# Optimization experiments

Hardware: AMD Instinct MI355X
Metric: run time of the kernel (lower is better)

The kernel has to match this reference:

```python
import jax, jax.numpy as jnp
import numpy as np

DIM = 768
N_HEADS = 12
HEAD_DIM = DIM // N_HEADS
HIDDEN = int(DIM * 4.0)
EPS = 1e-6


def setup_inputs() -> dict:
    key = jax.random.key(0)
    ks = jax.random.split(key, 12)
    s = 0.02
    return {
        "x": jax.random.normal(ks[0], (4, 2048, DIM), dtype=jnp.float32),
        "ln1_g": jnp.ones((DIM,), jnp.float32),
        "ln1_b": jnp.zeros((DIM,), jnp.float32),
        "qkv_w": jax.random.normal(ks[1], (3 * DIM, DIM), jnp.float32) * s,
        "qkv_b": jnp.zeros((3 * DIM,), jnp.float32),
        "proj_w": jax.random.normal(ks[2], (DIM, DIM), jnp.float32) * s,
        "proj_b": jnp.zeros((DIM,), jnp.float32),
        "ln2_g": jnp.ones((DIM,), jnp.float32),
        "ln2_b": jnp.zeros((DIM,), jnp.float32),
        "fc1_w": jax.random.normal(ks[3], (HIDDEN, DIM), jnp.float32) * s,
        "fc1_b": jnp.zeros((HIDDEN,), jnp.float32),
        "fc2_w": jax.random.normal(ks[4], (DIM, HIDDEN), jnp.float32) * s,
        "fc2_b": jnp.zeros((DIM,), jnp.float32),
    }


def layer_norm(x, g, b):
    mu = jnp.mean(x, axis=-1, keepdims=True)
    var = jnp.mean(jnp.square(x - mu), axis=-1, keepdims=True)
    return (x - mu) * jax.lax.rsqrt(var + EPS) * g + b


def reference(x, ln1_g, ln1_b, qkv_w, qkv_b, proj_w, proj_b,
              ln2_g, ln2_b, fc1_w, fc1_b, fc2_w, fc2_b):
    B, N, D = x.shape
    # --- attention branch ---
    h = layer_norm(x, ln1_g, ln1_b)
    qkv = h @ qkv_w.T + qkv_b                      # [B, N, 3D]
    qkv = qkv.reshape(B, N, 3, N_HEADS, HEAD_DIM).transpose(2, 0, 3, 1, 4)
    q, k, v = qkv[0], qkv[1], qkv[2]               # each [B, H, N, d]
    scale = HEAD_DIM ** -0.5
    scores = jnp.einsum("bhqd,bhkd->bhqk", q, k) * scale
    attn = jax.nn.softmax(scores, axis=-1)
    out = jnp.einsum("bhqk,bhkd->bhqd", attn, v)   # [B, H, N, d]
    out = out.transpose(0, 2, 1, 3).reshape(B, N, D)
    x = x + (out @ proj_w.T + proj_b)
    # --- MLP branch ---
    h = layer_norm(x, ln2_g, ln2_b)
    h = jax.nn.gelu(h @ fc1_w.T + fc1_b, approximate=False)
    x = x + (h @ fc2_w.T + fc2_b)
    return x
```

## Files before the change

### kernel.cpp

```cpp
#include <hip/hip_runtime.h>


#define DIM    768
#define NHEAD  12
#define HDIM   64
#define HID    3072
#define BATCH  4
#define SEQ    2048
#define MTOT   (BATCH * SEQ)
#define D3     (3 * DIM)

#define QSCALE 0.18033688011112042f
#define GELU_K 2.30220816f

typedef short bf16x8 __attribute__((ext_vector_type(8)));
typedef float f32x4  __attribute__((ext_vector_type(4)));

__device__ __forceinline__ float exp2fast(float x) {
    return __builtin_amdgcn_exp2f(x);
}

__device__ __forceinline__ float gelu_f(float v) {
    float y = v * (1.f + 0.044715f * v * v) * GELU_K;
    float t = exp2fast(fminf(y, 30.f));
#if __has_builtin(__builtin_amdgcn_rcpf)
    return v * t * __builtin_amdgcn_rcpf(t + 1.f);
#else
    return v * t / (t + 1.f);
#endif
}

__device__ __forceinline__ short f2bf(float f) {
    union { float f; unsigned u; } c; c.f = f;
    unsigned r = c.u + 0x7FFFu + ((c.u >> 16) & 1u);
    return (short)(r >> 16);
}

__device__ __forceinline__ short4 pk4bf(float a, float b, float c, float d) {
    int lo, hi;
    asm("v_cvt_pk_bf16_f32 %0, %1, %2" : "=v"(lo) : "v"(a), "v"(b));
    asm("v_cvt_pk_bf16_f32 %0, %1, %2" : "=v"(hi) : "v"(c), "v"(d));
    short4 r;
    *(int*)&r.x = lo; *(int*)&r.z = hi;
    return r;
}

__device__ __forceinline__ void gld_lds16(const short* g, short* l) {
    __builtin_amdgcn_global_load_lds(
        (const __attribute__((address_space(1))) unsigned int*)g,
        (__attribute__((address_space(3))) unsigned int*)l, 16, 0, 0);
}

__global__ __launch_bounds__(256) void tobf4_k(
    const float* __restrict__ s0, short* __restrict__ d0, int n0,
    const float* __restrict__ s1, short* __restrict__ d1, int n1,
    const float* __restrict__ s2, short* __restrict__ d2, int n2,
    const float* __restrict__ s3, short* __restrict__ d3, int n3)
{
    int i = blockIdx.x * 256 + threadIdx.x;
    const float* s; short* d;
    if (i < n0)                { s = s0; d = d0; }
    else if ((i -= n0) < n1)   { s = s1; d = d1; }
    else if ((i -= n1) < n2)   { s = s2; d = d2; }
    else if ((i -= n2) < n3)   { s = s3; d = d3; }
    else return;
    float4 v = ((const float4*)s)[i];
    ((short4*)d)[i] = pk4bf(v.x, v.y, v.z, v.w);
}

__global__ __launch_bounds__(256) void ln_k(
    const float* __restrict__ x, const float* __restrict__ g,
    const float* __restrict__ bta, short* __restrict__ y)
{
    __shared__ float sb[2][4];
    const int row = blockIdx.x, tid = threadIdx.x;
    const float* xr = x + (size_t)row * DIM;
    float v0 = xr[tid], v1 = xr[tid + 256], v2 = xr[tid + 512];
    float s = v0 + v1 + v2;
    #pragma unroll
    for (int o = 32; o; o >>= 1) s += __shfl_down(s, o);
    if ((tid & 63) == 0) sb[0][tid >> 6] = s;
    __syncthreads();
    float mu = (sb[0][0] + sb[0][1] + sb[0][2] + sb[0][3]) * (1.f / DIM);
    float d0 = v0 - mu, d1 = v1 - mu, d2 = v2 - mu;
    float q = d0 * d0 + d1 * d1 + d2 * d2;
    #pragma unroll
    for (int o = 32; o; o >>= 1) q += __shfl_down(q, o);
    if ((tid & 63) == 0) sb[1][tid >> 6] = q;
    __syncthreads();
    float var = (sb[1][0] + sb[1][1] + sb[1][2] + sb[1][3]) * (1.f / DIM);
    float inv = rsqrtf(var + 1e-6f);
    short* yr = y + (size_t)row * DIM;
    yr[tid]       = f2bf(d0 * inv * g[tid]       + bta[tid]);
    yr[tid + 256] = f2bf(d1 * inv * g[tid + 256] + bta[tid + 256]);
    yr[tid + 512] = f2bf(d2 * inv * g[tid + 512] + bta[tid + 512]);
}

template<int MODE>
__global__ __launch_bounds__(512) void gemmA_k(
    const short* __restrict__ A, const short* __restrict__ W,
    const float* __restrict__ bias,
    void* __restrict__ Cout, short* __restrict__ vt,
    int M, int N, int K)
{
    __shared__ __align__(16) short sm[2][28672];

    const int tid = threadIdx.x, lane = tid & 63, wv = tid >> 6;
    const int l15 = lane & 15, quad = lane >> 4;

    const int gx = gridDim.x;
    const int bid = blockIdx.y * gx + blockIdx.x;
    const int bm = (bid / gx) << 8;
    const int bn = (bid % gx) * 192;

    const int srow  = lane >> 3;
    const int chunk = (lane & 7) ^ srow;
    const int arow  = wv * 8 + srow;

    const short* Ag = A + (size_t)(bm + arow) * K + chunk * 8;
    const short* Wg = W + (size_t)(bn + arow) * K + chunk * 8;

    const int nt = K >> 6;

    auto stage = [&](short* s_, int k0) {
        #pragma unroll
        for (int i = 0; i < 4; ++i)
            gld_lds16(Ag + k0 + (size_t)(i * 64) * K,
                      s_ + i * 4096 + wv * 512);
        #pragma unroll
        for (int i = 0; i < 3; ++i)
            gld_lds16(Wg + k0 + (size_t)(i * 64) * K,
                      s_ + 16384 + i * 4096 + wv * 512);
    };

    f32x4 acc[4][6] = {};
    stage(&sm[0][0], 0);

    const int rsel = (wv >> 1) * 64;
    const int csel = (wv & 1) * 96;
    const int xorr = (l15 & 7) << 4;

    for (int t = 0; t < nt; ++t) {
        const char* Sc = (const char*)&sm[t & 1][0];
        asm volatile("s_waitcnt vmcnt(0)" ::: "memory");
        __builtin_amdgcn_s_barrier();
        __builtin_amdgcn_sched_barrier(0);
        if (t + 1 < nt) stage(&sm[(t + 1) & 1][0], (t + 1) << 6);

        #pragma unroll
        for (int ks = 0; ks < 2; ++ks) {
            bf16x8 af[4], bfr[6];
            const int kc = ((ks << 6) + (quad << 4)) ^ xorr;
            #pragma unroll
            for (int mf = 0; mf < 4; ++mf) {
                const int row = rsel + mf * 16 + l15;
                af[mf] = *(const bf16x8*)(Sc + (row << 7) + kc);
            }
            #pragma unroll
            for (int nf = 0; nf < 6; ++nf) {
                const int brow = csel + nf * 16 + l15;
                bfr[nf] = *(const bf16x8*)(Sc + 32768 + (brow << 7) + kc);
            }
            __builtin_amdgcn_s_setprio(1);
            #pragma unroll
            for (int mf = 0; mf < 4; ++mf)
                #pragma unroll
                for (int nf = 0; nf < 6; ++nf)
                    acc[mf][nf] = __builtin_amdgcn_mfma_f32_16x16x32_bf16(
                        af[mf], bfr[nf], acc[mf][nf], 0, 0, 0);
            __builtin_amdgcn_s_setprio(0);
        }
    }

    if (MODE == 3 && bn >= 1536) {
        const size_t bbase = (size_t)(bm >> 11) * NHEAD;
        #pragma unroll
        for (int nf = 0; nf < 6; ++nf) {
            const int col = bn + csel + nf * 16 + l15;
            const float bv = bias[col];
            const int d = col - 1536, hh = d >> 6, dd = d & 63;
            const size_t vrow = (((bbase + hh) << 6) + dd) * SEQ;
            #pragma unroll
            for (int mf = 0; mf < 4; ++mf) {
                const int n0 = (bm & 2047) + rsel + mf * 16 + (quad << 2);
                *(short4*)&vt[vrow + n0] =
                    pk4bf(acc[mf][nf][0] + bv, acc[mf][nf][1] + bv,
                          acc[mf][nf][2] + bv, acc[mf][nf][3] + bv);
            }
        }
        return;
    }

    #pragma unroll
    for (int nf = 0; nf < 6; ++nf) {
        const int col = bn + csel + nf * 16 + l15;
        const float bv = bias[col];
        #pragma unroll
        for (int mf = 0; mf < 4; ++mf) {
            const int row0 = bm + rsel + mf * 16 + (quad << 2);
            #pragma unroll
            for (int r = 0; r < 4; ++r) {
                float v = acc[mf][nf][r] + bv;
                const size_t idx = (size_t)(row0 + r) * N + col;
                if (MODE == 2) {
                    ((short*)Cout)[idx] = f2bf(gelu_f(v));
                } else {
                    if (col < DIM) v *= QSCALE;
                    ((short*)Cout)[idx] = f2bf(v);
                }
            }
        }
    }
}

template<int MODE>
__global__ __launch_bounds__(512) void gemm8_k(
    const short* __restrict__ A, const short* __restrict__ W,
    const float* __restrict__ bias, const float* __restrict__ resid,
    void* __restrict__ Cout, short* __restrict__ vt,
    int M, int N, int K)
{
    __shared__ __align__(16) short sm[3][20480];

    const int tid = threadIdx.x, lane = tid & 63, wv = tid >> 6;
    const int l15 = lane & 15, quad = lane >> 4;

    const int gx = gridDim.x;
    const int bid = blockIdx.y * gx + blockIdx.x;
    const int s = bid >> 3, xcd = bid & 7;
    const int st = ((s >> 5) << 3) + xcd;
    const int cell = s & 31, cy = cell >> 2, cx = cell & 3;
    const int nstx = gx >> 2;
    const int sty = st / nstx, stx = st - sty * nstx;
    const int bm = (((sty << 3) + cy) << 7);
    const int bn = ((stx << 2) + cx) * 192;

    const int srow  = lane >> 3;
    const int chunk = (lane & 7) ^ srow;
    const int arow  = wv * 8 + srow;

    const short* Ag = A + (size_t)(bm + arow) * K + chunk * 8;
    const short* Wg = W + (size_t)(bn + arow) * K + chunk * 8;

    const int nt = K >> 6;

    auto stage = [&](short* s_, int k0) {
        #pragma unroll
        for (int i = 0; i < 2; ++i)
            gld_lds16(Ag + k0 + (size_t)(i * 64) * K,
                      s_ + i * 4096 + wv * 512);
        #pragma unroll
        for (int i = 0; i < 3; ++i)
            gld_lds16(Wg + k0 + (size_t)(i * 64) * K,
                      s_ + 8192 + i * 4096 + wv * 512);
    };

    f32x4 acc[4][3] = {};
    stage(&sm[0][0], 0);
    stage(&sm[1][0], (nt > 1 ? 1 : 0) << 6);

    const int rsel = (wv >> 2) * 64;
    const int csel = (wv & 3) * 48;
    const int xorr = (l15 & 7) << 4;

    for (int t = 0; t < nt; ++t) {
        const char* Sc = (const char*)&sm[t % 3][0];
        asm volatile("s_waitcnt vmcnt(5)" ::: "memory");
        __builtin_amdgcn_s_barrier();
        __builtin_amdgcn_sched_barrier(0);
        const int kn = (t + 2 < nt ? t + 2 : nt - 1) << 6;
        stage(&sm[(t + 2) % 3][0], kn);

        #pragma unroll
        for (int ks = 0; ks < 2; ++ks) {
            bf16x8 af[4], bfr[3];
            const int kc = ((ks << 6) + (quad << 4)) ^ xorr;
            #pragma unroll
            for (int mf = 0; mf < 4; ++mf) {
                const int row = rsel + mf * 16 + l15;
                af[mf] = *(const bf16x8*)(Sc + (row << 7) + kc);
            }
            #pragma unroll
            for (int nf = 0; nf < 3; ++nf) {
                const int brow = csel + nf * 16 + l15;
                bfr[nf] = *(const bf16x8*)(Sc + 16384 + (brow << 7) + kc);
            }
            __builtin_amdgcn_s_setprio(1);
            #pragma unroll
            for (int mf = 0; mf < 4; ++mf)
                #pragma unroll
                for (int nf = 0; nf < 3; ++nf)
                    acc[mf][nf] = __builtin_amdgcn_mfma_f32_16x16x32_bf16(
                        af[mf], bfr[nf], acc[mf][nf], 0, 0, 0);
            __builtin_amdgcn_s_setprio(0);
        }
    }

    #pragma unroll
    for (int nf = 0; nf < 3; ++nf) {
        const int col = bn + csel + nf * 16 + l15;
        const float bv = bias[col];
        #pragma unroll
        for (int mf = 0; mf < 4; ++mf) {
            const int row0 = bm + rsel + mf * 16 + (quad << 2);
            #pragma unroll
            for (int r = 0; r < 4; ++r) {
                float v = acc[mf][nf][r] + bv;
                const size_t idx = (size_t)(row0 + r) * N + col;
                ((float*)Cout)[idx] = v + resid[idx];
            }
        }
    }
}

__global__ __launch_bounds__(256) void attn_k(
    const short* __restrict__ qkv, const short* __restrict__ vt,
    short* __restrict__ out)
{
    __shared__ __align__(16) short Ks[64][64];
    __shared__ __align__(16) short Vs[64][64];
    __shared__ __align__(16) short Ps[4][32][64];

    const int bh = blockIdx.x, b = bh / NHEAD, h = bh % NHEAD;
    const int qb = blockIdx.y;
    const int tid = threadIdx.x, lane = tid & 63, wv = tid >> 6;
    const int l15 = lane & 15, quad = lane >> 4;
    const int lsw = (l15 & 7) << 3;

    const size_t qbase = (size_t)b * SEQ * D3;
    const size_t vbase = (((size_t)bh) << 6) * SEQ;

    bf16x8 qf[2][2];
    #pragma unroll
    for (int tm = 0; tm < 2; ++tm) {
        const int m = (qb << 7) + wv * 32 + tm * 16 + l15;
        #pragma unroll
        for (int ks = 0; ks < 2; ++ks)
            qf[tm][ks] = *(const bf16x8*)&qkv[qbase + (size_t)m * D3 + h * HDIM
                                             + ks * 32 + (quad << 3)];
    }

    float psum[2] = {0.f, 0.f};
    f32x4 acc[2][4] = {};

    const int srow = tid >> 3;
    const int scol = (tid & 7) << 3;

    for (int kb = 0; kb < SEQ / 64; ++kb) {
        __syncthreads();
        #pragma unroll
        for (int p = 0; p < 2; ++p) {
            const int r = srow + p * 32;
            const int pc = scol ^ ((r & 7) << 3);
            *(int4*)&Ks[r][pc] = *(const int4*)&qkv[qbase
                + (size_t)((kb << 6) + r) * D3 + DIM + h * HDIM + scol];
            *(int4*)&Vs[r][pc] = *(const int4*)&vt[vbase
                + (size_t)r * SEQ + (kb << 6) + scol];
        }
        __syncthreads();

        f32x4 st[2][4] = {};
        __builtin_amdgcn_s_setprio(1);
        #pragma unroll
        for (int kt = 0; kt < 4; ++kt)
            #pragma unroll
            for (int ks = 0; ks < 2; ++ks) {
                bf16x8 kf = *(const bf16x8*)
                    &Ks[kt * 16 + l15][(ks * 32 + (quad << 3)) ^ lsw];
                #pragma unroll
                for (int tm = 0; tm < 2; ++tm)
                    st[tm][kt] = __builtin_amdgcn_mfma_f32_16x16x32_bf16(
                        kf, qf[tm][ks], st[tm][kt], 0, 0, 0);
            }
        __builtin_amdgcn_s_setprio(0);

        #pragma unroll
        for (int tm = 0; tm < 2; ++tm) {
            #pragma unroll
            for (int kt = 0; kt < 4; ++kt) {
                const float p0 = exp2fast(st[tm][kt][0]);
                const float p1 = exp2fast(st[tm][kt][1]);
                const float p2 = exp2fast(st[tm][kt][2]);
                const float p3 = exp2fast(st[tm][kt][3]);
                psum[tm] += (p0 + p1) + (p2 + p3);
                *(short4*)&Ps[wv][tm * 16 + l15]
                             [(kt * 16 + (quad << 2)) ^ lsw] =
                    pk4bf(p0, p1, p2, p3);
            }
        }

        #pragma unroll
        for (int ks = 0; ks < 2; ++ks) {
            bf16x8 pf[2];
            #pragma unroll
            for (int tm = 0; tm < 2; ++tm)
                pf[tm] = *(const bf16x8*)
                    &Ps[wv][tm * 16 + l15][(ks * 32 + (quad << 3)) ^ lsw];
            __builtin_amdgcn_s_setprio(1);
            #pragma unroll
            for (int u = 0; u < 4; ++u) {
                bf16x8 vf = *(const bf16x8*)
                    &Vs[u * 16 + l15][(ks * 32 + (quad << 3)) ^ lsw];
                #pragma unroll
                for (int tm = 0; tm < 2; ++tm)
                    acc[tm][u] = __builtin_amdgcn_mfma_f32_16x16x32_bf16(
                        vf, pf[tm], acc[tm][u], 0, 0, 0);
            }
            __builtin_amdgcn_s_setprio(0);
        }
    }

    #pragma unroll
    for (int tm = 0; tm < 2; ++tm) {
        psum[tm] += __shfl_xor(psum[tm], 16);
        psum[tm] += __shfl_xor(psum[tm], 32);
    }

    #pragma unroll
    for (int tm = 0; tm < 2; ++tm) {
        const float inv = 1.f / psum[tm];
        const int q = (qb << 7) + wv * 32 + tm * 16 + l15;
        #pragma unroll
        for (int u = 0; u < 4; ++u) {
            const int d0 = u * 16 + (quad << 2);
            *(short4*)&out[((size_t)b * SEQ + q) * DIM + h * HDIM + d0] =
                pk4bf(acc[tm][u][0] * inv, acc[tm][u][1] * inv,
                      acc[tm][u][2] * inv, acc[tm][u][3] * inv);
        }
    }
}

extern "C" void kernel_launch(void* const* d_in, const int* in_sizes, int n_in,
                              void* d_out, int out_size, void* d_ws, size_t ws_size,
                              hipStream_t stream) {
    const float* x      = (const float*)d_in[0];
    const float* ln1_g  = (const float*)d_in[1];
    const float* ln1_b  = (const float*)d_in[2];
    const float* qkv_w  = (const float*)d_in[3];
    const float* qkv_b  = (const float*)d_in[4];
    const float* proj_w = (const float*)d_in[5];
    const float* proj_b = (const float*)d_in[6];
    const float* ln2_g  = (const float*)d_in[7];
    const float* ln2_b  = (const float*)d_in[8];
    const float* fc1_w  = (const float*)d_in[9];
    const float* fc1_b  = (const float*)d_in[10];
    const float* fc2_w  = (const float*)d_in[11];
    const float* fc2_b  = (const float*)d_in[12];
    float* out = (float*)d_out;

    short* ws16 = (short*)d_ws;
    short* wqkv = ws16;
    short* wprj = wqkv + (size_t)D3 * DIM;
    short* wf1  = wprj + (size_t)DIM * DIM;
    short* wf2  = wf1  + (size_t)HID * DIM;
    short* h    = wf2  + (size_t)DIM * HID;
    short* big  = h    + (size_t)MTOT * DIM;
    short* vtb  = big  + (size_t)MTOT * HID;
    float* x2   = (float*)(vtb + (size_t)MTOT * DIM);

    dim3 blk(256);

    const int n0 = (D3 * DIM) / 4, n1 = (DIM * DIM) / 4,
              n2 = (HID * DIM) / 4, n3 = (DIM * HID) / 4;
    tobf4_k<<<(n0 + n1 + n2 + n3 + 255) / 256, blk, 0, stream>>>(
        qkv_w, wqkv, n0, proj_w, wprj, n1, fc1_w, wf1, n2, fc2_w, wf2, n3);

    ln_k<<<MTOT, blk, 0, stream>>>(x, ln1_g, ln1_b, h);
    gemmA_k<3><<<dim3(D3 / 192, MTOT / 256), 512, 0, stream>>>(
        h, wqkv, qkv_b, big, vtb, MTOT, D3, DIM);
    attn_k<<<dim3(BATCH * NHEAD, SEQ / 128), blk, 0, stream>>>(big, vtb, h);
    gemm8_k<0><<<dim3(DIM / 192, MTOT / 128), 512, 0, stream>>>(
        h, wprj, proj_b, x, x2, nullptr, MTOT, DIM, DIM);
    ln_k<<<MTOT, blk, 0, stream>>>(x2, ln2_g, ln2_b, vtb);
    gemmA_k<2><<<dim3(HID / 192, MTOT / 256), 512, 0, stream>>>(
        vtb, wf1, fc1_b, big, nullptr, MTOT, HID, DIM);
    gemm8_k<0><<<dim3(DIM / 192, MTOT / 128), 512, 0, stream>>>(
        big, wf2, fc2_b, x2, out, nullptr, MTOT, DIM, HID);
}
```

Before: 354.4 us.

## Switch GEMM to double-buffered LDS and register-prefetch attention K/V tiles

```diff
diff --git a/kernel.cpp b/kernel.cpp
--- a/kernel.cpp
+++ b/kernel.cpp
@@ -214,13 +214,13 @@
 }
 
 template<int MODE>
-__global__ __launch_bounds__(512) void gemm8_k(
+__global__ __launch_bounds__(512, 4) void gemm8_k(
     const short* __restrict__ A, const short* __restrict__ W,
     const float* __restrict__ bias, const float* __restrict__ resid,
     void* __restrict__ Cout, short* __restrict__ vt,
     int M, int N, int K)
 {
-    __shared__ __align__(16) short sm[3][20480];
+    __shared__ __align__(16) short sm[2][20480];
 
     const int tid = threadIdx.x, lane = tid & 63, wv = tid >> 6;
     const int l15 = lane & 15, quad = lane >> 4;
@@ -257,19 +257,17 @@
 
     f32x4 acc[4][3] = {};
     stage(&sm[0][0], 0);
-    stage(&sm[1][0], (nt > 1 ? 1 : 0) << 6);
 
     const int rsel = (wv >> 2) * 64;
     const int csel = (wv & 3) * 48;
     const int xorr = (l15 & 7) << 4;
 
     for (int t = 0; t < nt; ++t) {
-        const char* Sc = (const char*)&sm[t % 3][0];
-        asm volatile("s_waitcnt vmcnt(5)" ::: "memory");
+        const char* Sc = (const char*)&sm[t & 1][0];
+        asm volatile("s_waitcnt vmcnt(0)" ::: "memory");
         __builtin_amdgcn_s_barrier();
         __builtin_amdgcn_sched_barrier(0);
-        const int kn = (t + 2 < nt ? t + 2 : nt - 1) << 6;
-        stage(&sm[(t + 2) % 3][0], kn);
+        if (t + 1 < nt) stage(&sm[(t + 1) & 1][0], (t + 1) << 6);
 
         #pragma unroll
         for (int ks = 0; ks < 2; ++ks) {
@@ -346,16 +344,34 @@
     const int srow = tid >> 3;
     const int scol = (tid & 7) << 3;
 
+    int4 kreg[2], vreg[2];
+    #pragma unroll
+    for (int p = 0; p < 2; ++p) {
+        const int r = srow + p * 32;
+        kreg[p] = *(const int4*)&qkv[qbase + (size_t)r * D3 + DIM
+                                     + h * HDIM + scol];
+        vreg[p] = *(const int4*)&vt[vbase + (size_t)r * SEQ + scol];
+    }
+
     for (int kb = 0; kb < SEQ / 64; ++kb) {
         __syncthreads();
         #pragma unroll
         for (int p = 0; p < 2; ++p) {
             const int r = srow + p * 32;
             const int pc = scol ^ ((r & 7) << 3);
-            *(int4*)&Ks[r][pc] = *(const int4*)&qkv[qbase
-                + (size_t)((kb << 6) + r) * D3 + DIM + h * HDIM + scol];
-            *(int4*)&Vs[r][pc] = *(const int4*)&vt[vbase
-                + (size_t)r * SEQ + (kb << 6) + scol];
+            *(int4*)&Ks[r][pc] = kreg[p];
+            *(int4*)&Vs[r][pc] = vreg[p];
+        }
+        if (kb + 1 < SEQ / 64) {
+            #pragma unroll
+            for (int p = 0; p < 2; ++p) {
+                const int r = srow + p * 32;
+                kreg[p] = *(const int4*)&qkv[qbase
+                    + (size_t)(((kb + 1) << 6) + r) * D3 + DIM
+                    + h * HDIM + scol];
+                vreg[p] = *(const int4*)&vt[vbase
+                    + (size_t)r * SEQ + ((kb + 1) << 6) + scol];
+            }
         }
         __syncthreads();
 
```

Result: slower. 403.3 us (+13.8%).

## Double-buffer attention K/V via direct global-to-LDS loads; shrink GEMM to two stages

Applied to the files above, without the earlier changes.

```diff
diff --git a/kernel.cpp b/kernel.cpp
--- a/kernel.cpp
+++ b/kernel.cpp
@@ -214,13 +214,13 @@
 }
 
 template<int MODE>
-__global__ __launch_bounds__(512) void gemm8_k(
+__global__ __launch_bounds__(512, 4) void gemm8_k(
     const short* __restrict__ A, const short* __restrict__ W,
     const float* __restrict__ bias, const float* __restrict__ resid,
     void* __restrict__ Cout, short* __restrict__ vt,
     int M, int N, int K)
 {
-    __shared__ __align__(16) short sm[3][20480];
+    __shared__ __align__(16) short sm[2][20480];
 
     const int tid = threadIdx.x, lane = tid & 63, wv = tid >> 6;
     const int l15 = lane & 15, quad = lane >> 4;
@@ -257,19 +257,17 @@
 
     f32x4 acc[4][3] = {};
     stage(&sm[0][0], 0);
-    stage(&sm[1][0], (nt > 1 ? 1 : 0) << 6);
 
     const int rsel = (wv >> 2) * 64;
     const int csel = (wv & 3) * 48;
     const int xorr = (l15 & 7) << 4;
 
     for (int t = 0; t < nt; ++t) {
-        const char* Sc = (const char*)&sm[t % 3][0];
-        asm volatile("s_waitcnt vmcnt(5)" ::: "memory");
+        const char* Sc = (const char*)&sm[t & 1][0];
+        asm volatile("s_waitcnt vmcnt(0)" ::: "memory");
         __builtin_amdgcn_s_barrier();
         __builtin_amdgcn_sched_barrier(0);
-        const int kn = (t + 2 < nt ? t + 2 : nt - 1) << 6;
-        stage(&sm[(t + 2) % 3][0], kn);
+        if (t + 1 < nt) stage(&sm[(t + 1) & 1][0], (t + 1) << 6);
 
         #pragma unroll
         for (int ks = 0; ks < 2; ++ks) {
@@ -317,8 +315,8 @@
     const short* __restrict__ qkv, const short* __restrict__ vt,
     short* __restrict__ out)
 {
-    __shared__ __align__(16) short Ks[64][64];
-    __shared__ __align__(16) short Vs[64][64];
+    __shared__ __align__(16) short Ks[2][64][64];
+    __shared__ __align__(16) short Vs[2][64][64];
     __shared__ __align__(16) short Ps[4][32][64];
 
     const int bh = blockIdx.x, b = bh / NHEAD, h = bh % NHEAD;
@@ -343,21 +341,31 @@
     float psum[2] = {0.f, 0.f};
     f32x4 acc[2][4] = {};
 
-    const int srow = tid >> 3;
-    const int scol = (tid & 7) << 3;
+    const int rg  = lane >> 3;
+    const int gch = (lane & 7) ^ rg;
+
+    const short* Kg = qkv + qbase + (size_t)(wv * 16 + rg) * D3 + DIM
+                    + h * HDIM + gch * 8;
+    const short* Vg = vt + vbase + (size_t)(wv * 16 + rg) * SEQ + gch * 8;
+
+    auto stage = [&](int buf, int kb) {
+        #pragma unroll
+        for (int g = 0; g < 2; ++g) {
+            gld_lds16(Kg + (size_t)((kb << 6) + g * 8) * D3,
+                      &Ks[buf][wv * 16 + g * 8][0]);
+            gld_lds16(Vg + (size_t)(g * 8) * SEQ + (kb << 6),
+                      &Vs[buf][wv * 16 + g * 8][0]);
+        }
+    };
+
+    stage(0, 0);
 
     for (int kb = 0; kb < SEQ / 64; ++kb) {
-        __syncthreads();
-        #pragma unroll
-        for (int p = 0; p < 2; ++p) {
-            const int r = srow + p * 32;
-            const int pc = scol ^ ((r & 7) << 3);
-            *(int4*)&Ks[r][pc] = *(const int4*)&qkv[qbase
-                + (size_t)((kb << 6) + r) * D3 + DIM + h * HDIM + scol];
-            *(int4*)&Vs[r][pc] = *(const int4*)&vt[vbase
-                + (size_t)r * SEQ + (kb << 6) + scol];
-        }
-        __syncthreads();
+        const int cur = kb & 1;
+        asm volatile("s_waitcnt vmcnt(0)" ::: "memory");
+        __builtin_amdgcn_s_barrier();
+        __builtin_amdgcn_sched_barrier(0);
+        if (kb + 1 < SEQ / 64) stage(cur ^ 1, kb + 1);
 
         f32x4 st[2][4] = {};
         __builtin_amdgcn_s_setprio(1);
@@ -366,7 +374,7 @@
             #pragma unroll
             for (int ks = 0; ks < 2; ++ks) {
                 bf16x8 kf = *(const bf16x8*)
-                    &Ks[kt * 16 + l15][(ks * 32 + (quad << 3)) ^ lsw];
+                    &Ks[cur][kt * 16 + l15][(ks * 32 + (quad << 3)) ^ lsw];
                 #pragma unroll
                 for (int tm = 0; tm < 2; ++tm)
                     st[tm][kt] = __builtin_amdgcn_mfma_f32_16x16x32_bf16(
@@ -400,7 +408,7 @@
             #pragma unroll
             for (int u = 0; u < 4; ++u) {
                 bf16x8 vf = *(const bf16x8*)
-                    &Vs[u * 16 + l15][(ks * 32 + (quad << 3)) ^ lsw];
+                    &Vs[cur][u * 16 + l15][(ks * 32 + (quad << 3)) ^ lsw];
                 #pragma unroll
                 for (int tm = 0; tm < 2; ++tm)
                     acc[tm][u] = __builtin_amdgcn_mfma_f32_16x16x32_bf16(
```

New measurement: 372.3 us. 5.0% more time.
